# Kernel optimization log

Hardware: AMD Instinct MI355X
Metric: run time of the kernel (lower is better)

Reference implementation:

```python
import jax, jax.numpy as jnp
import numpy as np

B, S, D, H, KVH, HD, NREP = 1, 2048, 5120, 64, 8, 128, 8
CACHE_B, MAX_S = 32, 2048
EPS = 1e-6


def setup_inputs() -> dict:
    key = jax.random.key(0)
    ks = jax.random.split(key, 8)
    x = jax.random.normal(ks[0], (B, S, D), dtype=jnp.float32)
    # torch nn.Linear stores weight as [out_features, in_features]
    wq = jax.random.normal(ks[1], (H * HD, D), dtype=jnp.float32) * 0.02
    wk = jax.random.normal(ks[2], (KVH * HD, D), dtype=jnp.float32) * 0.02
    wv = jax.random.normal(ks[3], (KVH * HD, D), dtype=jnp.float32) * 0.02
    wo = jax.random.normal(ks[4], (D, H * HD), dtype=jnp.float32) * 0.02
    q_norm_w = jnp.ones((HD,), dtype=jnp.float32)
    k_norm_w = jnp.ones((HD,), dtype=jnp.float32)
    cache_k = jnp.zeros((CACHE_B, MAX_S, KVH, HD), dtype=jnp.float32)
    cache_v = jnp.zeros((CACHE_B, MAX_S, KVH, HD), dtype=jnp.float32)
    # rotary frequencies: theta = 10000^{-2i/d}
    inv_freq = 1.0 / (10000.0 ** (jnp.arange(0, HD, 2, dtype=jnp.float32) / HD))  # [64]
    angles = jnp.arange(S, dtype=jnp.float32)[:, None] * inv_freq[None, :]  # [S,64]
    freqs_cos = jnp.cos(angles)
    freqs_sin = jnp.sin(angles)
    # causal additive mask [S, S]
    mask = jnp.triu(jnp.full((S, S), -1e9, dtype=jnp.float32), k=1)
    return {
        "x": x, "wq": wq, "wk": wk, "wv": wv, "wo": wo,
        "q_norm_w": q_norm_w, "k_norm_w": k_norm_w,
        "cache_k": cache_k, "cache_v": cache_v,
        "freqs_cos": freqs_cos, "freqs_sin": freqs_sin,
        "mask": mask, "start_pos": 0,
    }


def _rmsnorm(v, w):
    vf = v.astype(jnp.float32)
    n = vf * jax.lax.rsqrt(jnp.mean(vf * vf, axis=-1, keepdims=True) + EPS)
    return n.astype(v.dtype) * w


def _rope(v, cos, sin):
    # v: [B,S,h,HD]; pairs (even, odd) rotated by angle per pair
    vr = v.reshape(*v.shape[:-1], HD // 2, 2)
    ve, vo = vr[..., 0], vr[..., 1]
    cos = cos[None, :, None, :]  # [1,S,1,64]
    sin = sin[None, :, None, :]
    oe = ve * cos - vo * sin
    oo = ve * sin + vo * cos
    return jnp.stack([oe, oo], axis=-1).reshape(v.shape)


def reference(x, wq, wk, wv, wo, q_norm_w, k_norm_w, cache_k, cache_v,
              freqs_cos, freqs_sin, mask, start_pos):
    bsz, seqlen, _ = x.shape
    xq = (x @ wq.T).reshape(bsz, seqlen, H, HD)
    xk = (x @ wk.T).reshape(bsz, seqlen, KVH, HD)
    xv = (x @ wv.T).reshape(bsz, seqlen, KVH, HD)
    xq = _rmsnorm(xq, q_norm_w)
    xk = _rmsnorm(xk, k_norm_w)
    xq = _rope(xq, freqs_cos, freqs_sin)
    xk = _rope(xk, freqs_cos, freqs_sin)
    # KV-cache append
    cache_k = jax.lax.dynamic_update_slice(cache_k, xk, (0, start_pos, 0, 0))
    cache_v = jax.lax.dynamic_update_slice(cache_v, xv, (0, start_pos, 0, 0))
    kv_len = start_pos + seqlen
    keys = cache_k[:bsz, :kv_len]    # [B,T,KVH,HD]
    values = cache_v[:bsz, :kv_len]
    # GQA expansion (repeat_interleave over kv heads)
    keys = jnp.repeat(keys, NREP, axis=2)      # [B,T,H,HD]
    values = jnp.repeat(values, NREP, axis=2)
    scores = jnp.einsum('bqhd,bkhd->bhqk', xq, keys) / np.float32(np.sqrt(HD))
    if mask is not None:
        scores = scores + mask[None, None, :, :]
    probs = jax.nn.softmax(scores.astype(jnp.float32), axis=-1).astype(xq.dtype)
    out = jnp.einsum('bhqk,bkhd->bqhd', probs, values)
    out = out.reshape(bsz, seqlen, H * HD)
    return out @ wo.T
```

## Files before the change

### kernel.cpp

```cpp
#include <hip/hip_runtime.h>

typedef unsigned short ushort_t;
typedef __attribute__((ext_vector_type(8))) short short8;
typedef __attribute__((ext_vector_type(4))) float f32x4;
typedef __attribute__((ext_vector_type(16))) float f32x16;

#define AS1U(p) ((const __attribute__((address_space(1))) unsigned int*)(p))
#define AS3U(p) ((__attribute__((address_space(3))) unsigned int*)(p))

__device__ __forceinline__ float bf2f(ushort_t u) {
  union { unsigned int i; float f; } v; v.i = ((unsigned int)u) << 16; return v.f;
}
__device__ __forceinline__ ushort_t f2bf(float f) {
  union { float f; unsigned int i; } v; v.f = f;
  unsigned int r = v.i + 0x7fffu + ((v.i >> 16) & 1u);
  return (ushort_t)(r >> 16);
}

template <int N>
__device__ __forceinline__ void waitvm() {
  if constexpr (N == 0) asm volatile("s_waitcnt vmcnt(0)" ::: "memory");
  else if constexpr (N == 2) asm volatile("s_waitcnt vmcnt(2)" ::: "memory");
  else if constexpr (N == 4) asm volatile("s_waitcnt vmcnt(4)" ::: "memory");
  else if constexpr (N == 5) asm volatile("s_waitcnt vmcnt(5)" ::: "memory");
  else if constexpr (N == 8) asm volatile("s_waitcnt vmcnt(8)" ::: "memory");
  else if constexpr (N == 10) asm volatile("s_waitcnt vmcnt(10)" ::: "memory");
}

#define PACK8(dst, S, base)                                                             \
  {                                                                                     \
    union { unsigned int u[4]; short8 s; } pk;                                          \
    asm("v_cvt_pk_bf16_f32 %0, %1, %2" : "=v"(pk.u[0]) : "v"(S[base + 0]), "v"(S[base + 1])); \
    asm("v_cvt_pk_bf16_f32 %0, %1, %2" : "=v"(pk.u[1]) : "v"(S[base + 2]), "v"(S[base + 3])); \
    asm("v_cvt_pk_bf16_f32 %0, %1, %2" : "=v"(pk.u[2]) : "v"(S[base + 4]), "v"(S[base + 5])); \
    asm("v_cvt_pk_bf16_f32 %0, %1, %2" : "=v"(pk.u[3]) : "v"(S[base + 6]), "v"(S[base + 7])); \
    dst = pk.s;                                                                         \
  }

__global__ void cvt_bf16(const float* __restrict__ src, ushort_t* __restrict__ dst, int n8) {
  int i = blockIdx.x * 256 + threadIdx.x;
  if (i >= n8) return;
  const float4* s4 = (const float4*)src;
  float4 a = s4[2 * i], b = s4[2 * i + 1];
  short8 u;
  u[0] = (short)f2bf(a.x); u[1] = (short)f2bf(a.y); u[2] = (short)f2bf(a.z); u[3] = (short)f2bf(a.w);
  u[4] = (short)f2bf(b.x); u[5] = (short)f2bf(b.y); u[6] = (short)f2bf(b.z); u[7] = (short)f2bf(b.w);
  *(short8*)(dst + (size_t)i * 8) = u;
}

template <int OUTF32, int MF, int NF>
__global__ __launch_bounds__(512, 2) void gemm8p(const ushort_t* __restrict__ A,
                                                 const ushort_t* __restrict__ B,
                                                 void* __restrict__ Cv,
                                                 int M, int N, int K) {
  constexpr int BM = MF * 32, BN = NF * 64;
  constexpr int LA = BM / 64, LB = BN / 64;
  constexpr int LMAX = (LA > LB) ? LA : LB;
  constexpr int ABUF = BM * 32;
  __shared__ __align__(16) ushort_t SH[4][(BM + BN) * 32];
  const int t = threadIdx.x;
  const int lane = t & 63, w = t >> 6;
  const int wm = w >> 2, wn = w & 3;
  const int r = lane & 15, g = lane >> 4;
  const int nwg = gridDim.x * gridDim.y;
  const int l = blockIdx.y * gridDim.x + blockIdx.x;
  const int wg = (l & 7) * (nwg >> 3) + (l >> 3);
  const int m0 = (wg & (gridDim.x - 1)) * BM, n0 = (wg / gridDim.x) * BN;
  const int NT = K >> 5;
  const int t256 = t & 255;

  const ushort_t* sp[LMAX];
  int sdst[LMAX];
  if (w < 4) {
#pragma unroll
    for (int i = 0; i < LA; ++i) {
      int s = t256 + i * 256;
      int row = s >> 2, c = s & 3;
      int csrc = c ^ ((row >> 1) & 3);
      sp[i] = A + (size_t)(m0 + row) * K + csrc * 8;
      sdst[i] = s * 8;
    }
  } else {
#pragma unroll
    for (int i = 0; i < LB; ++i) {
      int s = t256 + i * 256;
      int row = s >> 2, c = s & 3;
      int csrc = c ^ ((row >> 1) & 3);
      sp[i] = B + (size_t)(n0 + row) * K + csrc * 8;
      sdst[i] = ABUF + s * 8;
    }
  }
  auto STAGE = [&](int b) {
    if (w < 4) {
#pragma unroll
      for (int i = 0; i < LA; ++i) {
        __builtin_amdgcn_global_load_lds(AS1U(sp[i]), AS3U(&SH[b][0] + sdst[i]), 16, 0, 0);
        sp[i] += 32;
      }
    } else {
#pragma unroll
      for (int i = 0; i < LB; ++i) {
        __builtin_amdgcn_global_load_lds(AS1U(sp[i]), AS3U(&SH[b][0] + sdst[i]), 16, 0, 0);
        sp[i] += 32;
      }
    }
  };

  STAGE(0); STAGE(1); STAGE(2);
  if (w < 4) waitvm<2 * LA>(); else waitvm<2 * LB>();
  __builtin_amdgcn_s_barrier();

  f32x4 acc[MF][NF] = {};
  int bsel = 0;
  for (int tt = 0; tt < NT; ++tt) {
    const ushort_t* As = &SH[bsel][0];
    const ushort_t* Bs = &SH[bsel][ABUF];
    const int t3 = tt + 3;
    const int b3 = (bsel + 3) & 3;
    short8 bf[NF], af0[MF / 2], af1[MF / 2];

#pragma unroll
    for (int m = 0; m < MF / 2; ++m) {
      int row = wm * (MF * 16) + m * 16 + r;
      af0[m] = *(const short8*)(As + row * 32 + (g ^ ((row >> 1) & 3)) * 8);
    }
#pragma unroll
    for (int n = 0; n < NF; ++n) {
      int row = wn * (NF * 16) + n * 16 + r;
      bf[n] = *(const short8*)(Bs + row * 32 + (g ^ ((row >> 1) & 3)) * 8);
    }
    if (t3 < NT) STAGE(b3);
    __builtin_amdgcn_s_barrier();
    __builtin_amdgcn_s_setprio(1);
#pragma unroll
    for (int m = 0; m < MF / 2; ++m)
#pragma unroll
      for (int n = 0; n < NF; ++n)
        acc[m][n] = __builtin_amdgcn_mfma_f32_16x16x32_bf16(af0[m], bf[n], acc[m][n], 0, 0, 0);
    __builtin_amdgcn_s_setprio(0);

#pragma unroll
    for (int m = 0; m < MF / 2; ++m) {
      int row = wm * (MF * 16) + (MF / 2 + m) * 16 + r;
      af1[m] = *(const short8*)(As + row * 32 + (g ^ ((row >> 1) & 3)) * 8);
    }
    if (tt + 3 < NT) {
      if (w < 4) waitvm<2 * LA>(); else waitvm<2 * LB>();
    } else if (tt + 2 < NT) {
      if (w < 4) waitvm<LA>(); else waitvm<LB>();
    } else if (tt + 1 < NT) {
      waitvm<0>();
    }
    __builtin_amdgcn_s_barrier();
    __builtin_amdgcn_s_setprio(1);
#pragma unroll
    for (int m = 0; m < MF / 2; ++m)
#pragma unroll
      for (int n = 0; n < NF; ++n)
        acc[MF / 2 + m][n] = __builtin_amdgcn_mfma_f32_16x16x32_bf16(af1[m], bf[n], acc[MF / 2 + m][n], 0, 0, 0);
    __builtin_amdgcn_s_setprio(0);
    bsel = (bsel + 1) & 3;
  }

#pragma unroll
  for (int m = 0; m < MF; ++m)
#pragma unroll
    for (int n = 0; n < NF; ++n)
#pragma unroll
      for (int j = 0; j < 4; ++j) {
        int row = m0 + wm * (MF * 16) + m * 16 + g * 4 + j;
        int col = n0 + wn * (NF * 16) + n * 16 + r;
        if (OUTF32)
          ((float*)Cv)[(size_t)row * N + col] = acc[m][n][j];
        else
          ((ushort_t*)Cv)[(size_t)row * N + col] = f2bf(acc[m][n][j]);
      }
}

__global__ __launch_bounds__(256) void normrope(const ushort_t* __restrict__ qkv,
                                                const float* __restrict__ qw, const float* __restrict__ kw,
                                                const float* __restrict__ fc, const float* __restrict__ fs,
                                                ushort_t* __restrict__ Qb, ushort_t* __restrict__ Kb) {
  const int slot = blockIdx.x * 4 + (threadIdx.x >> 6);
  const int s = blockIdx.y, t = threadIdx.x & 63;
  const ushort_t* src;
  ushort_t* dst;
  const float* wn;
  float scale = 1.0f;
  if (slot < 64) {
    src = qkv + (size_t)s * 10240 + slot * 128;
    dst = Qb + ((size_t)slot * 2048 + s) * 128;
    wn = qw;
    scale = 0.08838834764831845f;
  } else {
    int kh = slot - 64;
    src = qkv + (size_t)s * 10240 + 8192 + kh * 128;
    dst = Kb + ((size_t)kh * 2048 + s) * 128;
    wn = kw;
  }
  float e0 = bf2f(src[2 * t]), e1 = bf2f(src[2 * t + 1]);
  float ss = e0 * e0 + e1 * e1;
#pragma unroll
  for (int m = 1; m < 64; m <<= 1) ss += __shfl_xor(ss, m);
  float rn = rsqrtf(ss * (1.0f / 128.0f) + 1e-6f);
  float v0 = e0 * rn * wn[2 * t], v1 = e1 * rn * wn[2 * t + 1];
  float c = fc[s * 64 + t], sn = fs[s * 64 + t];
  float oe = v0 * c - v1 * sn;
  float oo = v0 * sn + v1 * c;
  dst[2 * t] = f2bf(oe * scale);
  dst[2 * t + 1] = f2bf(oo * scale);
}

__global__ __launch_bounds__(256) void vtrans(const ushort_t* __restrict__ qkv,
                                              ushort_t* __restrict__ Vt) {
  __shared__ __align__(16) ushort_t T[64 * 128];
  const int t = threadIdx.x, st = blockIdx.x, kvh = blockIdx.y;
#pragma unroll
  for (int i = 0; i < 4; ++i) {
    int slot = t + i * 256;
    int srow = slot >> 4, c8 = slot & 15;
    short8 v = *(const short8*)(qkv + (size_t)(st * 64 + srow) * 10240 + 9216 + kvh * 128 + c8 * 8);
    int sw = (((srow & 7) ^ ((srow >> 3) & 7)) << 4);
    *(short8*)((char*)T + srow * 256 + ((c8 * 16) ^ sw)) = v;
  }
  __syncthreads();
#pragma unroll
  for (int i = 0; i < 4; ++i) {
    int slot = t + i * 256;
    int d = slot >> 3, s8 = slot & 7;
    short8 u;
#pragma unroll
    for (int j = 0; j < 8; ++j) {
      int row = s8 * 8 + j;
      int sw = (((row & 7) ^ ((row >> 3) & 7)) << 4);
      u[j] = *(const ushort_t*)((char*)T + row * 256 + ((d * 2) ^ sw));
    }
    *(short8*)(Vt + ((size_t)kvh * 128 + d) * 2048 + st * 64 + s8 * 8) = u;
  }
}

__global__ __launch_bounds__(256) void attn_fwd(const ushort_t* __restrict__ Qg,
                                                const ushort_t* __restrict__ Kg,
                                                const ushort_t* __restrict__ VtG,
                                                ushort_t* __restrict__ Og) {
  __shared__ __align__(16) ushort_t Ks[2][64 * 128];
  __shared__ __align__(16) ushort_t Vs[2][128 * 64];
  const int t = threadIdx.x, lane = t & 63, w = t >> 6;
  const int q5 = lane & 31, hi = lane >> 5;
  const int h = blockIdx.x, qt = (int)gridDim.y - 1 - (int)blockIdx.y, kvh = h >> 3;
  const int qrow0 = qt * 128 + w * 32;
  const int qglob = qrow0 + q5;

  const int pa = q5 & 3, pp = (q5 >> 2) & 1, pb = q5 >> 3;
  const int kr = (pb >> 1) * 16 + pp * 8 + (pb & 1) * 4 + pa;
  const int kswz = (kr & 7) << 4;
  const int swz = (q5 & 7) << 4;

  short8 qf[8];
#pragma unroll
  for (int ks = 0; ks < 8; ++ks)
    qf[ks] = *(const short8*)(Qg + ((size_t)h * 2048 + qglob) * 128 + ks * 16 + hi * 8);

  f32x16 o[4] = {};
  float mrun = -3.0e38f, lrun = 0.0f;

  const int kbmax_blk = 2 * qt + 1;
  const int kbmax_w = (qrow0 + 31) >> 6;

  auto STAGE = [&](int b, int kb) {
#pragma unroll
    for (int i = 0; i < 4; ++i) {
      int slot = t + i * 256;
      int kv = slot >> 4, c = slot & 15;
      int csrc = c ^ (kv & 7);
      __builtin_amdgcn_global_load_lds(AS1U(Kg + ((size_t)kvh * 2048 + kb * 64 + kv) * 128 + csrc * 8),
                                       AS3U(&Ks[b][0] + slot * 8), 16, 0, 0);
    }
#pragma unroll
    for (int i = 0; i < 4; ++i) {
      int slot = t + i * 256;
      int d = slot >> 3, c = slot & 7;
      int csrc = c ^ (d & 7);
      __builtin_amdgcn_global_load_lds(AS1U(VtG + ((size_t)kvh * 128 + d) * 2048 + kb * 64 + csrc * 8),
                                       AS3U(&Vs[b][0] + slot * 8), 16, 0, 0);
    }
  };

  STAGE(0, 0);
  int cur = 0;

  for (int kb = 0; kb <= kbmax_blk; ++kb) {
    asm volatile("s_waitcnt vmcnt(0)" ::: "memory");
    __syncthreads();
    if (kb < kbmax_blk) STAGE(cur ^ 1, kb + 1);

    if (kb <= kbmax_w) {
      const char* kbase = (const char*)&Ks[cur][0];
      const char* vbase = (const char*)&Vs[cur][0];

      f32x16 st0 = {}, st1 = {};
#pragma unroll
      for (int ks = 0; ks < 8; ++ks) {
        int cslot = ((ks * 2 + hi) * 16) ^ kswz;
        short8 kf0 = *(const short8*)(kbase + kr * 256 + cslot);
        short8 kf1 = *(const short8*)(kbase + (32 + kr) * 256 + cslot);
        __builtin_amdgcn_s_setprio(1);
        st0 = __builtin_amdgcn_mfma_f32_32x32x16_bf16(kf0, qf[ks], st0, 0, 0, 0);
        st1 = __builtin_amdgcn_mfma_f32_32x32x16_bf16(kf1, qf[ks], st1, 0, 0, 0);
        __builtin_amdgcn_s_setprio(0);
      }

      if (kb == kbmax_w) {
#pragma unroll
        for (int r = 0; r < 16; ++r) {
          int kv0 = kb * 64 + (r >> 3) * 16 + hi * 8 + (r & 7);
          if (kv0 > qglob) st0[r] = -1.0e30f;
          if (kv0 + 32 > qglob) st1[r] = -1.0e30f;
        }
      }

      float pmax = st0[0];
#pragma unroll
      for (int r = 1; r < 16; ++r) pmax = fmaxf(pmax, st0[r]);
#pragma unroll
      for (int r = 0; r < 16; ++r) pmax = fmaxf(pmax, st1[r]);
      pmax = fmaxf(pmax, __shfl_xor(pmax, 32));
      if (!__all(pmax <= mrun + 8.0f)) {
        float mn = fmaxf(mrun, pmax);
        float sc = __expf(mrun - mn);
        mrun = mn;
        lrun *= sc;
#pragma unroll
        for (int db = 0; db < 4; ++db) o[db] *= sc;
      }
      float rs = 0.0f;
#pragma unroll
      for (int r = 0; r < 16; ++r) { st0[r] = __expf(st0[r] - mrun); rs += st0[r]; }
#pragma unroll
      for (int r = 0; r < 16; ++r) { st1[r] = __expf(st1[r] - mrun); rs += st1[r]; }
      rs += __shfl_xor(rs, 32);
      lrun += rs;

      short8 pf[4];
      PACK8(pf[0], st0, 0);
      PACK8(pf[1], st0, 8);
      PACK8(pf[2], st1, 0);
      PACK8(pf[3], st1, 8);

#pragma unroll
      for (int db = 0; db < 4; ++db) {
#pragma unroll
        for (int ks = 0; ks < 4; ++ks) {
          short8 vf = *(const short8*)(vbase + (db * 32 + q5) * 128 + ((((ks * 2 + hi) * 16)) ^ swz));
          __builtin_amdgcn_s_setprio(1);
          o[db] = __builtin_amdgcn_mfma_f32_32x32x16_bf16(vf, pf[ks], o[db], 0, 0, 0);
          __builtin_amdgcn_s_setprio(0);
        }
      }
    }
    cur ^= 1;
  }

  __syncthreads();
  char* tr = ((char*)Ks) + w * 8192;
  float inv = 1.0f / lrun;
#pragma unroll
  for (int db = 0; db < 4; ++db)
#pragma unroll
    for (int r = 0; r < 16; r += 2) {
      unsigned int u;
      float lo = o[db][r] * inv, hiv = o[db][r + 1] * inv;
      asm("v_cvt_pk_bf16_f32 %0, %1, %2" : "=v"(u) : "v"(lo), "v"(hiv));
      int d = db * 32 + (r & 3) + 8 * (r >> 2) + 4 * hi;
      *(unsigned int*)(tr + q5 * 256 + ((d * 2) ^ swz)) = u;
    }
  asm volatile("s_waitcnt lgkmcnt(0)" ::: "memory");
#pragma unroll
  for (int p = 0; p < 8; ++p) {
    int row = (lane >> 3) + (p >> 1) * 8;
    int c = (lane & 7) + (p & 1) * 8;
    short8 v = *(const short8*)(tr + row * 256 + ((c * 16) ^ ((row & 7) << 4)));
    *(short8*)(Og + (size_t)(qrow0 + row) * 8192 + h * 128 + c * 8) = v;
  }
}

extern "C" void kernel_launch(void* const* d_in, const int* in_sizes, int n_in,
                              void* d_out, int out_size, void* d_ws, size_t ws_size,
                              hipStream_t stream) {
  const float* x = (const float*)d_in[0];
  const float* wq = (const float*)d_in[1];
  const float* wk = (const float*)d_in[2];
  const float* wv = (const float*)d_in[3];
  const float* wo = (const float*)d_in[4];
  const float* qw = (const float*)d_in[5];
  const float* kw = (const float*)d_in[6];
  const float* fc = (const float*)d_in[9];
  const float* fs = (const float*)d_in[10];

  char* ws = (char*)d_ws;
  ushort_t* Wb = (ushort_t*)(ws);
  ushort_t* qkv = (ushort_t*)(ws + 104857600);
  ushort_t* xb = (ushort_t*)(ws + 146800640);
  ushort_t* Qb = xb;
  ushort_t* Kb = (ushort_t*)(ws + 180355072);
  ushort_t* Vtb = (ushort_t*)(ws + 184549376);
  ushort_t* attnb = qkv;

  {
    int n8 = 2048 * 5120 / 8;
    cvt_bf16<<<dim3((n8 + 255) / 256), 256, 0, stream>>>(x, xb, n8);
  }
  {
    int n8 = 8192 * 5120 / 8;
    cvt_bf16<<<dim3((n8 + 255) / 256), 256, 0, stream>>>(wq, Wb, n8);
  }
  {
    int n8 = 1024 * 5120 / 8;
    cvt_bf16<<<dim3((n8 + 255) / 256), 256, 0, stream>>>(wk, Wb + (size_t)8192 * 5120, n8);
    cvt_bf16<<<dim3((n8 + 255) / 256), 256, 0, stream>>>(wv, Wb + (size_t)9216 * 5120, n8);
  }

  gemm8p<0, 8, 5><<<dim3(8, 32), 512, 0, stream>>>(xb, Wb, qkv, 2048, 10240, 5120);

  {
    int n8 = 5120 * 8192 / 8;
    cvt_bf16<<<dim3((n8 + 255) / 256), 256, 0, stream>>>(wo, Wb, n8);
  }

  normrope<<<dim3(18, 2048), 256, 0, stream>>>(qkv, qw, kw, fc, fs, Qb, Kb);

  vtrans<<<dim3(32, 8), 256, 0, stream>>>(qkv, Vtb);

  attn_fwd<<<dim3(64, 16), 256, 0, stream>>>(Qb, Kb, Vtb, attnb);

  gemm8p<1, 4, 5><<<dim3(16, 16), 512, 0, stream>>>(attnb, Wb, (float*)d_out, 2048, 5120, 8192);
}
```

Before: 648.9 us.

## Fuse fp32-to-bf16 weight conversion into GEMM B-operand staging

Drops the separate conversion kernels for wq, wk, wv and wo. The GEMM now reads fp32 weights directly, picking among three source pointers by row range, and the B-loading waves convert to bf16 in registers before writing to LDS. The A operand still uses async global-to-LDS loads. This removes a full extra pass that read fp32 weights and wrote bf16 copies to the workspace. In exchange, each GEMM tile fetches twice the bytes for B, repeated across M tiles, and goes through register-staged loads with explicit waits, which may lengthen the GEMM main loop.

```diff
diff --git a/kernel.cpp b/kernel.cpp
--- a/kernel.cpp
+++ b/kernel.cpp
@@ -22,9 +22,7 @@
   if constexpr (N == 0) asm volatile("s_waitcnt vmcnt(0)" ::: "memory");
   else if constexpr (N == 2) asm volatile("s_waitcnt vmcnt(2)" ::: "memory");
   else if constexpr (N == 4) asm volatile("s_waitcnt vmcnt(4)" ::: "memory");
-  else if constexpr (N == 5) asm volatile("s_waitcnt vmcnt(5)" ::: "memory");
   else if constexpr (N == 8) asm volatile("s_waitcnt vmcnt(8)" ::: "memory");
-  else if constexpr (N == 10) asm volatile("s_waitcnt vmcnt(10)" ::: "memory");
 }
 
 #define PACK8(dst, S, base)                                                             \
@@ -49,13 +47,15 @@
 }
 
 template <int OUTF32, int MF, int NF>
-__global__ __launch_bounds__(512, 2) void gemm8p(const ushort_t* __restrict__ A,
-                                                 const ushort_t* __restrict__ B,
-                                                 void* __restrict__ Cv,
-                                                 int M, int N, int K) {
+__global__ __launch_bounds__(512, 2) void gemmF(const ushort_t* __restrict__ A,
+                                                const float* __restrict__ B0,
+                                                const float* __restrict__ B1,
+                                                const float* __restrict__ B2,
+                                                int r1, int r2,
+                                                void* __restrict__ Cv,
+                                                int M, int N, int K) {
   constexpr int BM = MF * 32, BN = NF * 64;
   constexpr int LA = BM / 64, LB = BN / 64;
-  constexpr int LMAX = (LA > LB) ? LA : LB;
   constexpr int ABUF = BM * 32;
   __shared__ __align__(16) ushort_t SH[4][(BM + BN) * 32];
   const int t = threadIdx.x;
@@ -69,16 +69,19 @@
   const int NT = K >> 5;
   const int t256 = t & 255;
 
-  const ushort_t* sp[LMAX];
-  int sdst[LMAX];
+  const ushort_t* spA[LA];
+  int sdstA[LA];
+  const float* spB[LB];
+  int sdstB[LB];
+  float4 breg[LB][2];
   if (w < 4) {
 #pragma unroll
     for (int i = 0; i < LA; ++i) {
       int s = t256 + i * 256;
       int row = s >> 2, c = s & 3;
       int csrc = c ^ ((row >> 1) & 3);
-      sp[i] = A + (size_t)(m0 + row) * K + csrc * 8;
-      sdst[i] = s * 8;
+      spA[i] = A + (size_t)(m0 + row) * K + csrc * 8;
+      sdstA[i] = s * 8;
     }
   } else {
 #pragma unroll
@@ -86,28 +89,51 @@
       int s = t256 + i * 256;
       int row = s >> 2, c = s & 3;
       int csrc = c ^ ((row >> 1) & 3);
-      sp[i] = B + (size_t)(n0 + row) * K + csrc * 8;
-      sdst[i] = ABUF + s * 8;
-    }
-  }
-  auto STAGE = [&](int b) {
-    if (w < 4) {
-#pragma unroll
-      for (int i = 0; i < LA; ++i) {
-        __builtin_amdgcn_global_load_lds(AS1U(sp[i]), AS3U(&SH[b][0] + sdst[i]), 16, 0, 0);
-        sp[i] += 32;
-      }
-    } else {
-#pragma unroll
-      for (int i = 0; i < LB; ++i) {
-        __builtin_amdgcn_global_load_lds(AS1U(sp[i]), AS3U(&SH[b][0] + sdst[i]), 16, 0, 0);
-        sp[i] += 32;
-      }
+      int gr = n0 + row;
+      const float* bp;
+      if (gr < r1) bp = B0 + (size_t)gr * K;
+      else if (gr < r2) bp = B1 + (size_t)(gr - r1) * K;
+      else bp = B2 + (size_t)(gr - r2) * K;
+      spB[i] = bp + csrc * 8;
+      sdstB[i] = ABUF + s * 8;
+    }
+  }
+  auto STAGEA = [&](int b) {
+#pragma unroll
+    for (int i = 0; i < LA; ++i) {
+      __builtin_amdgcn_global_load_lds(AS1U(spA[i]), AS3U(&SH[b][0] + sdstA[i]), 16, 0, 0);
+      spA[i] += 32;
     }
   };
-
-  STAGE(0); STAGE(1); STAGE(2);
-  if (w < 4) waitvm<2 * LA>(); else waitvm<2 * LB>();
+  auto BLOAD = [&]() {
+#pragma unroll
+    for (int i = 0; i < LB; ++i) {
+      breg[i][0] = *(const float4*)(spB[i]);
+      breg[i][1] = *(const float4*)(spB[i] + 4);
+      spB[i] += 32;
+    }
+  };
+  auto BWRITE = [&](int b) {
+#pragma unroll
+    for (int i = 0; i < LB; ++i) {
+      union { unsigned int u[4]; short8 s; } pk;
+      asm("v_cvt_pk_bf16_f32 %0, %1, %2" : "=v"(pk.u[0]) : "v"(breg[i][0].x), "v"(breg[i][0].y));
+      asm("v_cvt_pk_bf16_f32 %0, %1, %2" : "=v"(pk.u[1]) : "v"(breg[i][0].z), "v"(breg[i][0].w));
+      asm("v_cvt_pk_bf16_f32 %0, %1, %2" : "=v"(pk.u[2]) : "v"(breg[i][1].x), "v"(breg[i][1].y));
+      asm("v_cvt_pk_bf16_f32 %0, %1, %2" : "=v"(pk.u[3]) : "v"(breg[i][1].z), "v"(breg[i][1].w));
+      *(short8*)(&SH[b][0] + sdstB[i]) = pk.s;
+    }
+  };
+
+  if (w < 4) {
+    STAGEA(0); STAGEA(1); STAGEA(2);
+    waitvm<2 * LA>();
+  } else {
+    BLOAD(); waitvm<0>(); BWRITE(0);
+    BLOAD(); waitvm<0>(); BWRITE(1);
+    BLOAD();
+    asm volatile("s_waitcnt lgkmcnt(0)" ::: "memory");
+  }
   __builtin_amdgcn_s_barrier();
 
   f32x4 acc[MF][NF] = {};
@@ -129,7 +155,12 @@
       int row = wn * (NF * 16) + n * 16 + r;
       bf[n] = *(const short8*)(Bs + row * 32 + (g ^ ((row >> 1) & 3)) * 8);
     }
-    if (t3 < NT) STAGE(b3);
+    if (w < 4) {
+      if (t3 < NT) STAGEA(b3);
+    } else {
+      if (tt + 2 < NT) { waitvm<0>(); BWRITE((bsel + 2) & 3); }
+      if (t3 < NT) BLOAD();
+    }
     __builtin_amdgcn_s_barrier();
     __builtin_amdgcn_s_setprio(1);
 #pragma unroll
@@ -144,12 +175,12 @@
       int row = wm * (MF * 16) + (MF / 2 + m) * 16 + r;
       af1[m] = *(const short8*)(As + row * 32 + (g ^ ((row >> 1) & 3)) * 8);
     }
-    if (tt + 3 < NT) {
-      if (w < 4) waitvm<2 * LA>(); else waitvm<2 * LB>();
-    } else if (tt + 2 < NT) {
-      if (w < 4) waitvm<LA>(); else waitvm<LB>();
-    } else if (tt + 1 < NT) {
-      waitvm<0>();
+    if (w < 4) {
+      if (tt + 3 < NT) waitvm<2 * LA>();
+      else if (tt + 2 < NT) waitvm<LA>();
+      else if (tt + 1 < NT) waitvm<0>();
+    } else {
+      asm volatile("s_waitcnt lgkmcnt(0)" ::: "memory");
     }
     __builtin_amdgcn_s_barrier();
     __builtin_amdgcn_s_setprio(1);
@@ -398,7 +429,6 @@
   const float* fs = (const float*)d_in[10];
 
   char* ws = (char*)d_ws;
-  ushort_t* Wb = (ushort_t*)(ws);
   ushort_t* qkv = (ushort_t*)(ws + 104857600);
   ushort_t* xb = (ushort_t*)(ws + 146800640);
   ushort_t* Qb = xb;
@@ -410,22 +440,9 @@
     int n8 = 2048 * 5120 / 8;
     cvt_bf16<<<dim3((n8 + 255) / 256), 256, 0, stream>>>(x, xb, n8);
   }
-  {
-    int n8 = 8192 * 5120 / 8;
-    cvt_bf16<<<dim3((n8 + 255) / 256), 256, 0, stream>>>(wq, Wb, n8);
-  }
-  {
-    int n8 = 1024 * 5120 / 8;
-    cvt_bf16<<<dim3((n8 + 255) / 256), 256, 0, stream>>>(wk, Wb + (size_t)8192 * 5120, n8);
-    cvt_bf16<<<dim3((n8 + 255) / 256), 256, 0, stream>>>(wv, Wb + (size_t)9216 * 5120, n8);
-  }
-
-  gemm8p<0, 8, 5><<<dim3(8, 32), 512, 0, stream>>>(xb, Wb, qkv, 2048, 10240, 5120);
-
-  {
-    int n8 = 5120 * 8192 / 8;
-    cvt_bf16<<<dim3((n8 + 255) / 256), 256, 0, stream>>>(wo, Wb, n8);
-  }
+
+  gemmF<0, 8, 5><<<dim3(8, 32), 512, 0, stream>>>(xb, wq, wk, wv, 8192, 9216,
+                                                  qkv, 2048, 10240, 5120);
 
   normrope<<<dim3(18, 2048), 256, 0, stream>>>(qkv, qw, kw, fc, fs, Qb, Kb);
 
@@ -433,5 +450,6 @@
 
   attn_fwd<<<dim3(64, 16), 256, 0, stream>>>(Qb, Kb, Vtb, attnb);
 
-  gemm8p<1, 4, 5><<<dim3(16, 16), 512, 0, stream>>>(attnb, Wb, (float*)d_out, 2048, 5120, 8192);
-}
+  gemmF<1, 4, 5><<<dim3(16, 16), 512, 0, stream>>>(attnb, wo, wo, wo, 1 << 30, 1 << 30,
+                                                   (float*)d_out, 2048, 5120, 8192);
+}
```

New measurement: 915.1 us. 41.0% more time.
